# Performance work log

Hardware: AMD Instinct MI355X
Metric: run time of the kernel (lower is better)

Reference implementation:

```python
import jax, jax.numpy as jnp
import numpy as np

L, B, T, H = 2, 512, 4096, 3


def _gru_layer(x, h0, Wih, Whh, bih, bhh):
    # x: [B,T,H], h0: [B,H], Wih/Whh: [3H,H], bih/bhh: [3H]
    gi = jnp.einsum('bth,gh->btg', x, Wih) + bih  # [B,T,3H] input projections

    def step(h, gi_t):
        gh = h @ Whh.T + bhh                      # [B,3H]
        i_r, i_z, i_n = jnp.split(gi_t, 3, axis=-1)
        h_r, h_z, h_n = jnp.split(gh, 3, axis=-1)
        r = jax.nn.sigmoid(i_r + h_r)
        z = jax.nn.sigmoid(i_z + h_z)
        n = jnp.tanh(i_n + r * h_n)
        h_new = (1.0 - z) * n + z * h
        return h_new, h_new

    h_last, ys = jax.lax.scan(step, h0, jnp.swapaxes(gi, 0, 1))  # ys: [T,B,H]
    return jnp.swapaxes(ys, 0, 1), h_last


def setup_inputs() -> dict:
    key = jax.random.key(0)
    ks = jax.random.split(key, 7)
    s = 0.3  # roughly torch's uniform(-1/sqrt(H), 1/sqrt(H)) scale
    return {
        'x': jax.random.normal(ks[0], (B, T, H), jnp.float32),
        'h': jnp.zeros((L, B, H), jnp.float32),
        'W_ih': jax.random.normal(ks[1], (L, 3 * H, H), jnp.float32) * s,
        'W_hh': jax.random.normal(ks[2], (L, 3 * H, H), jnp.float32) * s,
        'b_ih': jax.random.normal(ks[3], (L, 3 * H), jnp.float32) * s,
        'b_hh': jax.random.normal(ks[4], (L, 3 * H), jnp.float32) * s,
        'W_dec': jax.random.normal(ks[5], (1, H), jnp.float32) * s,
        'b_dec': jax.random.normal(ks[6], (1,), jnp.float32) * s,
    }


def reference(x, h, W_ih, W_hh, b_ih, b_hh, W_dec, b_dec):
    hs = []
    out = x
    for l in range(L):  # small fixed layer count
        out, h_l = _gru_layer(out, h[l], W_ih[l], W_hh[l], b_ih[l], b_hh[l])
        hs.append(h_l)
    h_out = jnp.stack(hs, axis=0)          # [L,B,H]
    y = out @ W_dec.T + b_dec              # [B,T,1]
    return (y, h_out)
```

## Files before the change

kernel.cpp:

```cpp
#include <hip/hip_runtime.h>


constexpr int T = 4096;
constexpr int B = 512;
constexpr float LOG2E = 1.44269504088896340736f;

__device__ __forceinline__ float fexp2(float v) { return __builtin_amdgcn_exp2f(v); }
__device__ __forceinline__ float frcp(float v)  { return __builtin_amdgcn_rcpf(v); }

template<int CTRL>
__device__ __forceinline__ float dppf(float v) {
    return __int_as_float(
        __builtin_amdgcn_update_dpp(0, __float_as_int(v), CTRL, 0xF, 0xF, true));
}

__device__ __forceinline__ float dpp_sel(float xv, float hbv) {
    return __int_as_float(__builtin_amdgcn_update_dpp(
        __float_as_int(xv), __float_as_int(hbv), 0x114, 0xF, 0xA, false));
}

#define GRU_IT(MODE, X0, X1, X2, YV) do {                                      \
    float hb0 = dppf<0x00>(h), hb1 = dppf<0x55>(h), hb2 = dppf<0xAA>(h);       \
    float in0 = dpp_sel((X0), hb0);                                            \
    float in1 = dpp_sel((X1), hb1);                                            \
    float in2 = dpp_sel((X2), hb2);                                            \
    YV = fmaf(wd2, hb2, fmaf(wd1, hb1, fmaf(wd0, hb0, bd)));                   \
    float crx = fmaf(wir2, in2, fmaf(wir1, in1, fmaf(wir0, in0, br)));         \
    float crh = fmaf(whr2, hb2, fmaf(whr1, hb1, whr0 * hb0));                  \
    float cr  = crx + crh;                                                     \
    float czx = fmaf(wiz2, in2, fmaf(wiz1, in1, fmaf(wiz0, in0, bz)));         \
    float czh = fmaf(whz2, hb2, fmaf(whz1, hb1, whz0 * hb0));                  \
    float cz  = czx + czh;                                                     \
    float gh  = fmaf(whn2, hb2, fmaf(whn1, hb1, fmaf(whn0, hb0, bnh)));        \
    float gi  = fmaf(win2, in2, fmaf(win1, in1, fmaf(win0, in0, bni)));        \
    float Er  = fexp2(cr);                                                     \
    float rr  = frcp(1.0f + Er);                                               \
    float aa  = fmaf(rr, gh, gi);                                              \
    float F   = fexp2(aa);                                                     \
    float Ez  = fexp2(cz);                                                     \
    float Fp  = F + 1.0f;                                                      \
    float Fm  = F - 1.0f;                                                      \
    float Ezp = Ez + 1.0f;                                                     \
    float num = fmaf(h, Fp, Ez * Fm);                  \
    float hn  = num * frcp(Fp * Ezp);                                          \
    if ((MODE) == 0)      h = hn;                                              \
    else if ((MODE) == 1) h = is_q0 ? hn : h;                                  \
    else                  h = is_q0 ? h : hn;                                  \
} while (0)

__global__ __launch_bounds__(64, 1)
void gru_pipe(const float* __restrict__ x,
              const float* __restrict__ h0,
              const float* __restrict__ Wih,
              const float* __restrict__ Whh,
              const float* __restrict__ bih,
              const float* __restrict__ bhh,
              const float* __restrict__ Wdec,
              const float* __restrict__ bdec,
              float* __restrict__ out)
{
    const int lane  = threadIdx.x;
    const int g8    = lane & 7;
    const int layer = (g8 >> 2) & 1;
    const int jj    = g8 & 3;
    const int j     = jj > 2 ? 2 : jj;
    const bool dummy = (jj == 3);
    const bool is_q0 = (layer == 0);
    const int b = (blockIdx.x * 64 + lane) >> 3;

    const float zm = dummy ? 0.0f : 1.0f;
    const float sR = -LOG2E * zm, sN = 2.0f * LOG2E * zm;
    const float* Wi = Wih + layer * 27;
    const float* Wh = Whh + layer * 27;
    const float* bi = bih + layer * 9;
    const float* bh = bhh + layer * 9;

    const float wir0 = Wi[j*3+0]*sR, wir1 = Wi[j*3+1]*sR, wir2 = Wi[j*3+2]*sR;
    const float wiz0 = Wi[(3+j)*3+0]*sR, wiz1 = Wi[(3+j)*3+1]*sR, wiz2 = Wi[(3+j)*3+2]*sR;
    const float win0 = Wi[(6+j)*3+0]*sN, win1 = Wi[(6+j)*3+1]*sN, win2 = Wi[(6+j)*3+2]*sN;
    const float whr0 = Wh[j*3+0]*sR, whr1 = Wh[j*3+1]*sR, whr2 = Wh[j*3+2]*sR;
    const float whz0 = Wh[(3+j)*3+0]*sR, whz1 = Wh[(3+j)*3+1]*sR, whz2 = Wh[(3+j)*3+2]*sR;
    const float whn0 = Wh[(6+j)*3+0]*sN, whn1 = Wh[(6+j)*3+1]*sN, whn2 = Wh[(6+j)*3+2]*sN;
    const float br  = (bi[j] + bh[j]) * sR;
    const float bz  = (bi[3+j] + bh[3+j]) * sR;
    const float bni = bi[6+j] * sN;
    const float bnh = bh[6+j] * sN;
    const float wd0 = Wdec[0], wd1 = Wdec[1], wd2 = Wdec[2], bd = bdec[0];

    float h = dummy ? 0.0f : h0[layer * B * 3 + b * 3 + j];

    const float4* xb = reinterpret_cast<const float4*>(x + (size_t)b * T * 3);
    float* yo = out + (size_t)b * T;

    float4 nx0 = xb[0], nx1 = xb[1], nx2 = xb[2];
    float4 cu0 = xb[3], cu1 = xb[4], cu2 = xb[5];
    float y0, y1, y2, y3, p2, p3;

    {
        GRU_IT(1, nx0.x, nx0.y, nx0.z, y0);
        GRU_IT(0, nx0.w, nx1.x, nx1.y, y1);
        GRU_IT(0, nx1.z, nx1.w, nx2.x, y2);
        GRU_IT(0, nx2.y, nx2.z, nx2.w, y3);
        p2 = y2; p3 = y3;
    }
    nx0 = xb[6]; nx1 = xb[7]; nx2 = xb[8];

    #pragma unroll 1
    for (int tc = 1; tc <= 1021; tc += 2) {
        const float4* pfa = xb + (tc + 2) * 3;
        float4 La0 = pfa[0], La1 = pfa[1], La2 = pfa[2];
        GRU_IT(0, cu0.x, cu0.y, cu0.z, y0);
        GRU_IT(0, cu0.w, cu1.x, cu1.y, y1);
        GRU_IT(0, cu1.z, cu1.w, cu2.x, y2);
        GRU_IT(0, cu2.y, cu2.z, cu2.w, y3);
        if (g8 == 7) {
            float4 q; q.x = p2; q.y = p3; q.z = y0; q.w = y1;
            *(float4*)(yo + 4 * tc - 4) = q;
        }
        p2 = y2; p3 = y3;
        const float4* pfb = xb + (((tc + 3) & 1023) * 3);
        float4 Lb0 = pfb[0], Lb1 = pfb[1], Lb2 = pfb[2];
        GRU_IT(0, nx0.x, nx0.y, nx0.z, y0);
        GRU_IT(0, nx0.w, nx1.x, nx1.y, y1);
        GRU_IT(0, nx1.z, nx1.w, nx2.x, y2);
        GRU_IT(0, nx2.y, nx2.z, nx2.w, y3);
        if (g8 == 7) {
            float4 q; q.x = p2; q.y = p3; q.z = y0; q.w = y1;
            *(float4*)(yo + 4 * tc) = q;
        }
        p2 = y2; p3 = y3;
        cu0 = La0; cu1 = La1; cu2 = La2;
        nx0 = Lb0; nx1 = Lb1; nx2 = Lb2;
    }

    GRU_IT(0, cu0.x, cu0.y, cu0.z, y0);
    GRU_IT(0, cu0.w, cu1.x, cu1.y, y1);
    GRU_IT(0, cu1.z, cu1.w, cu2.x, y2);
    GRU_IT(0, cu2.y, cu2.z, cu2.w, y3);
    if (g8 == 7) {
        float4 q; q.x = p2; q.y = p3; q.z = y0; q.w = y1;
        *(float4*)(yo + 4088) = q;
    }
    p2 = y2; p3 = y3;

    GRU_IT(2, 0.0f, 0.0f, 0.0f, y0);
    {
        float hb0 = dppf<0x00>(h), hb1 = dppf<0x55>(h), hb2 = dppf<0xAA>(h);
        y1 = fmaf(wd2, hb2, fmaf(wd1, hb1, fmaf(wd0, hb0, bd)));
    }
    if (g8 == 7) {
        float4 q; q.x = p2; q.y = p3; q.z = y0; q.w = y1;
        *(float4*)(yo + 4092) = q;
    }

    if (!dummy) out[B * T + (layer * B + b) * 3 + j] = h;
}

extern "C" void kernel_launch(void* const* d_in, const int* in_sizes, int n_in,
                              void* d_out, int out_size, void* d_ws, size_t ws_size,
                              hipStream_t stream) {
    const float* x    = (const float*)d_in[0];
    const float* h0   = (const float*)d_in[1];
    const float* Wih  = (const float*)d_in[2];
    const float* Whh  = (const float*)d_in[3];
    const float* bih  = (const float*)d_in[4];
    const float* bhh  = (const float*)d_in[5];
    const float* Wdec = (const float*)d_in[6];
    const float* bdec = (const float*)d_in[7];
    float* out = (float*)d_out;

    gru_pipe<<<(B * 8) / 64, 64, 0, stream>>>(x, h0, Wih, Whh, bih, bhh,
                                              Wdec, bdec, out);
}
```

Baseline: 484.4 us.

## Spread each batch row over 16 lanes, splitting r/z and n gates across lane pairs

Each batch row now uses 16 lanes instead of 8. Paired quads compute the r and z gates and the input and hidden halves of the n gate separately, then exchange partial results with DPP row operations. A dedicated lane evaluates the decoder output. The aim is to shorten the per-step dependent chain of transcendental operations by computing one sigmoid per lane and fusing the update algebra. The cost is twice as many lanes and waves, plus extra DPP cross-lane moves on the critical path.

```diff
diff --git a/kernel.cpp b/kernel.cpp
--- a/kernel.cpp
+++ b/kernel.cpp
@@ -13,39 +13,38 @@
     return __int_as_float(
         __builtin_amdgcn_update_dpp(0, __float_as_int(v), CTRL, 0xF, 0xF, true));
 }
-
-__device__ __forceinline__ float dpp_sel(float xv, float hbv) {
+template<int CTRL, int BANK>
+__device__ __forceinline__ float dppm(float oldv, float src) {
     return __int_as_float(__builtin_amdgcn_update_dpp(
-        __float_as_int(xv), __float_as_int(hbv), 0x114, 0xF, 0xA, false));
+        __float_as_int(oldv), __float_as_int(src), CTRL, 0xF, BANK, false));
 }
 
 #define GRU_IT(MODE, X0, X1, X2, YV) do {                                      \
-    float hb0 = dppf<0x00>(h), hb1 = dppf<0x55>(h), hb2 = dppf<0xAA>(h);       \
-    float in0 = dpp_sel((X0), hb0);                                            \
-    float in1 = dpp_sel((X1), hb1);                                            \
-    float in2 = dpp_sel((X2), hb2);                                            \
-    YV = fmaf(wd2, hb2, fmaf(wd1, hb1, fmaf(wd0, hb0, bd)));                   \
-    float crx = fmaf(wir2, in2, fmaf(wir1, in1, fmaf(wir0, in0, br)));         \
-    float crh = fmaf(whr2, hb2, fmaf(whr1, hb1, whr0 * hb0));                  \
-    float cr  = crx + crh;                                                     \
-    float czx = fmaf(wiz2, in2, fmaf(wiz1, in1, fmaf(wiz0, in0, bz)));         \
-    float czh = fmaf(whz2, hb2, fmaf(whz1, hb1, whz0 * hb0));                  \
-    float cz  = czx + czh;                                                     \
-    float gh  = fmaf(whn2, hb2, fmaf(whn1, hb1, fmaf(whn0, hb0, bnh)));        \
-    float gi  = fmaf(win2, in2, fmaf(win1, in1, fmaf(win0, in0, bni)));        \
-    float Er  = fexp2(cr);                                                     \
-    float rr  = frcp(1.0f + Er);                                               \
-    float aa  = fmaf(rr, gh, gi);                                              \
+    float b0 = dppf<0x00>(h), b1 = dppf<0x55>(h), b2 = dppf<0xAA>(h);          \
+    b0 = dppm<0x114, 0xA>(b0, b0);                  \
+    b1 = dppm<0x114, 0xA>(b1, b1);                                             \
+    b2 = dppm<0x114, 0xA>(b2, b2);                                             \
+    float in0 = dppm<0x118, 0xC>((X0), b0);          \
+    float in1 = dppm<0x118, 0xC>((X1), b1);                                    \
+    float in2 = dppm<0x118, 0xC>((X2), b2);                                    \
+    float cx  = fmaf(uA2, in2, fmaf(uA1, in1, fmaf(uA0, in0, bA)));            \
+    float chh = fmaf(vA2, b2, fmaf(vA1, b1, vA0 * b0));                        \
+    float c   = cx + chh;                   \
+    YV = c;                                                                    \
+    float gx  = fmaf(uB2, in2, fmaf(uB1, in1, fmaf(uB0, in0, bB)));            \
+    float ghh = fmaf(vB2, b2, fmaf(vB1, b1, vB0 * b0));                        \
+    float g   = gx + ghh;                          \
+    float E   = fexp2(c);                             \
+    float w   = frcp(1.0f + E);                       \
+    float m   = w * g;                                        \
+    float mm  = dppm<0x141, 0x5>(m, m);     \
+    float aa  = mm + g;                              \
     float F   = fexp2(aa);                                                     \
-    float Ez  = fexp2(cz);                                                     \
-    float Fp  = F + 1.0f;                                                      \
-    float Fm  = F - 1.0f;                                                      \
-    float Ezp = Ez + 1.0f;                                                     \
-    float num = fmaf(h, Fp, Ez * Fm);                  \
-    float hn  = num * frcp(Fp * Ezp);                                          \
+    float nn  = fmaf(-2.0f, frcp(F + 1.0f), 1.0f);                   \
+    float hn  = fmaf(w, h - nn, nn);                            \
     if ((MODE) == 0)      h = hn;                                              \
-    else if ((MODE) == 1) h = is_q0 ? hn : h;                                  \
-    else                  h = is_q0 ? h : hn;                                  \
+    else if ((MODE) == 1) h = is_L0 ? hn : h;                                  \
+    else                  h = is_L0 ? h : hn;                                  \
 } while (0)
 
 __global__ __launch_bounds__(64, 1)
@@ -60,34 +59,49 @@
               float* __restrict__ out)
 {
     const int lane  = threadIdx.x;
-    const int g8    = lane & 7;
-    const int layer = (g8 >> 2) & 1;
-    const int jj    = g8 & 3;
-    const int j     = jj > 2 ? 2 : jj;
-    const bool dummy = (jj == 3);
-    const bool is_q0 = (layer == 0);
-    const int b = (blockIdx.x * 64 + lane) >> 3;
+    const int g16   = lane & 15;
+    const int quad  = g16 >> 2;
+    const int layer = quad >> 1;
+    const bool ownr = (quad & 1) == 0;
+    const int kk    = g16 & 3;
+    const bool isdec = (g16 == 11);
+    const bool is_L0 = (g16 < 8);
+    const bool dlane = isdec;
+    const int b = (blockIdx.x * 64 + lane) >> 4;
 
-    const float zm = dummy ? 0.0f : 1.0f;
-    const float sR = -LOG2E * zm, sN = 2.0f * LOG2E * zm;
+    const int  uj    = ownr ? (kk < 3 ? kk : 0) : (kk > 0 ? 3 - kk : 0);
+    const bool valid = ownr ? (kk < 3) : (kk > 0);
+    const float zm = valid ? 1.0f : 0.0f;
+    const float sR = -LOG2E * zm;
+    const float sN = 2.0f * LOG2E * zm;
+
     const float* Wi = Wih + layer * 27;
     const float* Wh = Whh + layer * 27;
     const float* bi = bih + layer * 9;
     const float* bh = bhh + layer * 9;
 
-    const float wir0 = Wi[j*3+0]*sR, wir1 = Wi[j*3+1]*sR, wir2 = Wi[j*3+2]*sR;
-    const float wiz0 = Wi[(3+j)*3+0]*sR, wiz1 = Wi[(3+j)*3+1]*sR, wiz2 = Wi[(3+j)*3+2]*sR;
-    const float win0 = Wi[(6+j)*3+0]*sN, win1 = Wi[(6+j)*3+1]*sN, win2 = Wi[(6+j)*3+2]*sN;
-    const float whr0 = Wh[j*3+0]*sR, whr1 = Wh[j*3+1]*sR, whr2 = Wh[j*3+2]*sR;
-    const float whz0 = Wh[(3+j)*3+0]*sR, whz1 = Wh[(3+j)*3+1]*sR, whz2 = Wh[(3+j)*3+2]*sR;
-    const float whn0 = Wh[(6+j)*3+0]*sN, whn1 = Wh[(6+j)*3+1]*sN, whn2 = Wh[(6+j)*3+2]*sN;
-    const float br  = (bi[j] + bh[j]) * sR;
-    const float bz  = (bi[3+j] + bh[3+j]) * sR;
-    const float bni = bi[6+j] * sN;
-    const float bnh = bh[6+j] * sN;
-    const float wd0 = Wdec[0], wd1 = Wdec[1], wd2 = Wdec[2], bd = bdec[0];
+    const int rA = ownr ? (3 + uj) : uj;
+    float uA0 = Wi[rA*3+0]*sR, uA1 = Wi[rA*3+1]*sR, uA2 = Wi[rA*3+2]*sR;
+    float vA0 = Wh[rA*3+0]*sR, vA1 = Wh[rA*3+1]*sR, vA2 = Wh[rA*3+2]*sR;
+    float bA  = (bi[rA] + bh[rA]) * sR;
+    const int rN = 6 + uj;
+    float uB0, uB1, uB2, vB0, vB1, vB2, bB;
+    if (ownr) {
+        uB0 = Wi[rN*3+0]*sN; uB1 = Wi[rN*3+1]*sN; uB2 = Wi[rN*3+2]*sN;
+        vB0 = 0.0f; vB1 = 0.0f; vB2 = 0.0f;
+        bB  = bi[rN]*sN;
+    } else {
+        uB0 = 0.0f; uB1 = 0.0f; uB2 = 0.0f;
+        vB0 = Wh[rN*3+0]*sN; vB1 = Wh[rN*3+1]*sN; vB2 = Wh[rN*3+2]*sN;
+        bB  = bh[rN]*sN;
+    }
+    if (isdec) {
+        uA0 = uA1 = uA2 = 0.0f;
+        vA0 = Wdec[0]; vA1 = Wdec[1]; vA2 = Wdec[2];
+        bA  = bdec[0];
+    }
 
-    float h = dummy ? 0.0f : h0[layer * B * 3 + b * 3 + j];
+    float h = (ownr && kk < 3) ? h0[layer * B * 3 + b * 3 + kk] : 0.0f;
 
     const float4* xb = reinterpret_cast<const float4*>(x + (size_t)b * T * 3);
     float* yo = out + (size_t)b * T;
@@ -113,7 +127,7 @@
         GRU_IT(0, cu0.w, cu1.x, cu1.y, y1);
         GRU_IT(0, cu1.z, cu1.w, cu2.x, y2);
         GRU_IT(0, cu2.y, cu2.z, cu2.w, y3);
-        if (g8 == 7) {
+        if (dlane) {
             float4 q; q.x = p2; q.y = p3; q.z = y0; q.w = y1;
             *(float4*)(yo + 4 * tc - 4) = q;
         }
@@ -124,7 +138,7 @@
         GRU_IT(0, nx0.w, nx1.x, nx1.y, y1);
         GRU_IT(0, nx1.z, nx1.w, nx2.x, y2);
         GRU_IT(0, nx2.y, nx2.z, nx2.w, y3);
-        if (g8 == 7) {
+        if (dlane) {
             float4 q; q.x = p2; q.y = p3; q.z = y0; q.w = y1;
             *(float4*)(yo + 4 * tc) = q;
         }
@@ -137,7 +151,7 @@
     GRU_IT(0, cu0.w, cu1.x, cu1.y, y1);
     GRU_IT(0, cu1.z, cu1.w, cu2.x, y2);
     GRU_IT(0, cu2.y, cu2.z, cu2.w, y3);
-    if (g8 == 7) {
+    if (dlane) {
         float4 q; q.x = p2; q.y = p3; q.z = y0; q.w = y1;
         *(float4*)(yo + 4088) = q;
     }
@@ -145,15 +159,15 @@
 
     GRU_IT(2, 0.0f, 0.0f, 0.0f, y0);
     {
-        float hb0 = dppf<0x00>(h), hb1 = dppf<0x55>(h), hb2 = dppf<0xAA>(h);
-        y1 = fmaf(wd2, hb2, fmaf(wd1, hb1, fmaf(wd0, hb0, bd)));
+        float b0 = dppf<0x00>(h), b1 = dppf<0x55>(h), b2 = dppf<0xAA>(h);
+        y1 = fmaf(vA2, b2, fmaf(vA1, b1, fmaf(vA0, b0, bA)));
     }
-    if (g8 == 7) {
+    if (dlane) {
         float4 q; q.x = p2; q.y = p3; q.z = y0; q.w = y1;
         *(float4*)(yo + 4092) = q;
     }
 
-    if (!dummy) out[B * T + (layer * B + b) * 3 + j] = h;
+    if (ownr && kk < 3) out[B * T + (layer * B + b) * 3 + kk] = h;
 }
 
 extern "C" void kernel_launch(void* const* d_in, const int* in_sizes, int n_in,
@@ -169,6 +183,6 @@
     const float* bdec = (const float*)d_in[7];
     float* out = (float*)d_out;
 
-    gru_pipe<<<(B * 8) / 64, 64, 0, stream>>>(x, h0, Wih, Whh, bih, bhh,
-                                              Wdec, bdec, out);
+    gru_pipe<<<(B * 16) / 64, 64, 0, stream>>>(x, h0, Wih, Whh, bih, bhh,
+                                               Wdec, bdec, out);
 }
```

Result: faster. 457.8 us (-5.5%).
